# Optimization experiments

Hardware: AMD Instinct MI355X
Metric: run time of the kernel (lower is better)

The kernel has to match this reference:

```python
import jax, jax.numpy as jnp
import numpy as np

EPS = 1e-5
NEG = jnp.float32(-1e30)


def _mha(q_in, kv, in_w, in_b, out_w, out_b, n_heads, allowed=None):
    # torch nn.MultiheadAttention (batch_first, eval mode)
    B, Nq, D = q_in.shape
    hd = D // n_heads
    wq, wk, wv = jnp.split(in_w, 3, axis=0)
    bq, bk, bv = jnp.split(in_b, 3)
    q = (q_in @ wq.T + bq).reshape(B, Nq, n_heads, hd).transpose(0, 2, 1, 3)
    k = (kv @ wk.T + bk).reshape(B, -1, n_heads, hd).transpose(0, 2, 1, 3)
    v = (kv @ wv.T + bv).reshape(B, -1, n_heads, hd).transpose(0, 2, 1, 3)
    s = jnp.einsum('bhqd,bhkd->bhqk', q, k) / jnp.sqrt(jnp.float32(hd))
    if allowed is not None:
        s = jnp.where(allowed[:, None, :, :], s, NEG)
    a = jax.nn.softmax(s, axis=-1)
    o = jnp.einsum('bhqk,bhkd->bhqd', a, v).transpose(0, 2, 1, 3).reshape(B, Nq, D)
    o = o @ out_w.T + out_b
    if allowed is not None:
        # rows with no allowed keys: torch would NaN; we zero them (deterministic)
        o = jnp.where(allowed.any(-1)[..., None], o, 0.0)
    return o


def _layernorm(x, g, b):
    mu = x.mean(-1, keepdims=True)
    var = ((x - mu) ** 2).mean(-1, keepdims=True)
    return (x - mu) * jax.lax.rsqrt(var + EPS) * g + b


def setup_inputs() -> dict:
    key = jax.random.key(0)
    B, N, D, NH = 128, 128, 512, 8
    ks = jax.random.split(key, 16)
    s = 0.02
    return {
        'H': jax.random.normal(ks[0], (B, N, D), jnp.float32),
        'pred_heads': jax.random.randint(ks[1], (B, N), 0, N, jnp.int32),
        'mask': jnp.ones((B, N), jnp.int32),
        'head_in_w': jax.random.normal(ks[2], (3 * D, D)) * s,
        'head_in_b': jnp.zeros((3 * D,), jnp.float32),
        'head_out_w': jax.random.normal(ks[3], (D, D)) * s,
        'head_out_b': jnp.zeros((D,), jnp.float32),
        'sib_in_w': jax.random.normal(ks[4], (3 * D, D)) * s,
        'sib_in_b': jnp.zeros((3 * D,), jnp.float32),
        'sib_out_w': jax.random.normal(ks[5], (D, D)) * s,
        'sib_out_b': jnp.zeros((D,), jnp.float32),
        'child_w': jax.random.normal(ks[6], (D, 2 * D)) * s,
        'child_b': jnp.zeros((D,), jnp.float32),
        'gate_w': jax.random.normal(ks[7], (D, 4 * D)) * s,
        'gate_b': jnp.zeros((D,), jnp.float32),
        'trans_w': jax.random.normal(ks[8], (D, 4 * D)) * s,
        'trans_b': jnp.zeros((D,), jnp.float32),
        'ln_g': jnp.ones((D,), jnp.float32),
        'ln_b': jnp.zeros((D,), jnp.float32),
    }


def reference(H, pred_heads, mask, head_in_w, head_in_b, head_out_w, head_out_b,
              sib_in_w, sib_in_b, sib_out_w, sib_out_b, child_w, child_b,
              gate_w, gate_b, trans_w, trans_b, ln_g, ln_b):
    B, N, D = H.shape
    NH = 8
    heads = jnp.clip(pred_heads, 0, N - 1)  # [B,N]
    maskb = mask.astype(bool)

    # 1) head message: gather each node's head repr, attend Q=H, K=V=head_repr
    head_repr = jnp.take_along_axis(H, heads[..., None], axis=1)  # [B,N,D]
    head_msg = _mha(H, head_repr, head_in_w, head_in_b, head_out_w, head_out_b, NH)

    # 2) child aggregation: vectorized scatter-add replacing the Python loop.
    # loop runs d in [1, length) with mask a prefix -> valid = mask & (d >= 1)
    valid = maskb & (jnp.arange(N) >= 1)  # [B,N]
    contrib = H * valid[..., None].astype(H.dtype)
    flat_idx = (jnp.arange(B)[:, None] * N + heads).reshape(-1)
    child_sum = jnp.zeros((B * N, D), H.dtype).at[flat_idx].add(
        contrib.reshape(B * N, D)).reshape(B, N, D)
    child_count = jnp.zeros((B * N,), H.dtype).at[flat_idx].add(
        valid.reshape(-1).astype(H.dtype)).reshape(B, N, 1)
    child_avg = child_sum / jnp.maximum(child_count, 1.0)
    child_msg = jax.nn.gelu(
        jnp.concatenate([H, child_avg], -1) @ child_w.T + child_b,
        approximate=False)

    # 3) sibling attention (N <= 128 branch): same head, not self, both masked-in
    same_head = heads[:, :, None] == heads[:, None, :]
    eye = jnp.eye(N, dtype=bool)[None]
    allowed = same_head & ~eye & maskb[:, None, :] & maskb[:, :, None]
    sib_msg = _mha(H, H, sib_in_w, sib_in_b, sib_out_w, sib_out_b, NH, allowed=allowed)

    # 4) gated fusion + residual + layernorm
    combined = jnp.concatenate([H, head_msg, child_msg, sib_msg], -1)
    gate = jax.nn.sigmoid(combined @ gate_w.T + gate_b)
    update = jax.nn.gelu(combined @ trans_w.T + trans_b, approximate=False)
    return _layernorm(H + gate * update, ln_g, ln_b)
```

## Files before the change

kernel.cpp:

```cpp
#include <hip/hip_runtime.h>
#include <hip/hip_bf16.h>

typedef __bf16 bf16x8 __attribute__((ext_vector_type(8)));
typedef float f32x4 __attribute__((ext_vector_type(4)));

__device__ __forceinline__ void gload16(const void* g, void* l) {
  __builtin_amdgcn_global_load_lds(
      (const __attribute__((address_space(1))) unsigned int*)g,
      (__attribute__((address_space(3))) unsigned int*)l, 16, 0, 0);
}

__device__ __forceinline__ float gelu_f(float x) {
  return 0.5f * x * (1.f + erff(x * 0.70710678118654752f));
}
__device__ __forceinline__ float sigmoid_f(float x) {
  return 1.f / (1.f + __expf(-x));
}

template<int EPI>
__global__ __launch_bounds__(512, 2)
void gemm8_kernel(const __hip_bfloat16* __restrict__ A0, int lda0,
                  const __hip_bfloat16* __restrict__ A1, int lda1,
                  const __hip_bfloat16* __restrict__ A2, int lda2,
                  int ks1, int ks2,
                  const __hip_bfloat16* __restrict__ B, int ldb,
                  const float* __restrict__ bias,
                  const float* __restrict__ fvec,
                  const float* __restrict__ flags,
                  void* __restrict__ C, int ldc, int K)
{
  extern __shared__ __align__(16) char lds[];
  const int t = threadIdx.x;
  const int l = t & 63;
  const int w = t >> 6;
  const int l15 = l & 15, lg = (l >> 4) & 3;
  const int orig = blockIdx.y * gridDim.x + blockIdx.x;
  const int nwg = gridDim.x * gridDim.y;
  const int gy = gridDim.y;
  const int xcd = orig & 7, rk = orig >> 3, q = nwg >> 3, r = nwg & 7;
  const int bid = (xcd < r ? xcd * (q + 1) : r * (q + 1) + (xcd - r) * q) + rk;
  const int m0 = (bid % gy) * 256;
  const int n0 = (bid / gy) * 256;

  const int srow = t >> 2;
  const int kc8 = ((t & 3) ^ ((t >> 3) & 3)) * 8;
  const int mbase = (w >> 2) * 128;
  const int nbase = (w & 3) * 64;
  const int swz = (l15 >> 1) & 3;
  const int kslot = (lg ^ swz) * 8;
  int aoff[8], boff[4];
#pragma unroll
  for (int mf = 0; mf < 8; ++mf) aoff[mf] = (mbase + mf * 16 + l15) * 32 + kslot;
#pragma unroll
  for (int nf = 0; nf < 4; ++nf) boff[nf] = (nbase + nf * 16 + l15) * 32 + kslot;

  auto segA = [&](int k0, const __hip_bfloat16*& Ap, int& ldA, int& krel) {
    if (k0 >= ks2)      { Ap = A2; ldA = lda2; krel = k0 - ks2; }
    else if (k0 >= ks1) { Ap = A1; ldA = lda1; krel = k0 - ks1; }
    else                { Ap = A0; ldA = lda0; krel = k0; }
  };
  auto stageA = [&](int buf, const __hip_bfloat16* Ap, int ldA, int krel) {
    char* base = lds + buf * 32768 + t * 16;
    gload16(Ap + (size_t)(m0 + srow) * ldA + krel + kc8, base);
    gload16(Ap + (size_t)(m0 + 128 + srow) * ldA + krel + kc8, base + 8192);
  };
  auto stageB = [&](int buf, int k0) {
    char* base = lds + buf * 32768 + 16384 + t * 16;
    gload16(B + (size_t)(n0 + srow) * ldb + k0 + kc8, base);
    gload16(B + (size_t)(n0 + 128 + srow) * ldb + k0 + kc8, base + 8192);
  };

  f32x4 acc[8][4] = {};
  const int NT = K >> 5;

#pragma unroll 1
  for (int pt = 0; pt < 3; ++pt) {
    const __hip_bfloat16* Ap; int ldA, krel;
    segA(pt * 32, Ap, ldA, krel);
    stageA(pt, Ap, ldA, krel);
    stageB(pt, pt * 32);
  }
  asm volatile("s_waitcnt vmcnt(8)" ::: "memory");
  __builtin_amdgcn_s_barrier();
  __builtin_amdgcn_sched_barrier(0);

#pragma unroll 1
  for (int tt = 0; tt < NT; ++tt) {
    const int buf = tt & 3;
    const __hip_bfloat16* As = (const __hip_bfloat16*)(lds + buf * 32768);
    const __hip_bfloat16* Bs = (const __hip_bfloat16*)(lds + buf * 32768 + 16384);
    const int pf = tt + 3;
    const bool do_pf = pf < NT;
    const int pbuf = pf & 3;
    const __hip_bfloat16* Ap = A0; int ldA = lda0, krel = 0;
    if (do_pf) segA(pf * 32, Ap, ldA, krel);

    bf16x8 bv[4], av[4];
#pragma unroll
    for (int nf = 0; nf < 4; ++nf) bv[nf] = *(const bf16x8*)(Bs + boff[nf]);
#pragma unroll
    for (int mf = 0; mf < 4; ++mf) av[mf] = *(const bf16x8*)(As + aoff[mf]);
    if (do_pf) stageA(pbuf, Ap, ldA, krel);
    __builtin_amdgcn_s_setprio(1);
#pragma unroll
    for (int mf = 0; mf < 4; ++mf)
#pragma unroll
      for (int nf = 0; nf < 4; ++nf)
        acc[mf][nf] = __builtin_amdgcn_mfma_f32_16x16x32_bf16(av[mf], bv[nf], acc[mf][nf], 0, 0, 0);
    __builtin_amdgcn_s_setprio(0);

#pragma unroll
    for (int mf = 0; mf < 4; ++mf) av[mf] = *(const bf16x8*)(As + aoff[mf + 4]);
    if (do_pf) stageB(pbuf, pf * 32);
    __builtin_amdgcn_s_setprio(1);
#pragma unroll
    for (int mf = 0; mf < 4; ++mf)
#pragma unroll
      for (int nf = 0; nf < 4; ++nf)
        acc[mf + 4][nf] = __builtin_amdgcn_mfma_f32_16x16x32_bf16(av[mf], bv[nf], acc[mf + 4][nf], 0, 0, 0);
    __builtin_amdgcn_s_setprio(0);

    __builtin_amdgcn_sched_barrier(0);
    if (tt + 3 < NT)      asm volatile("s_waitcnt vmcnt(8)" ::: "memory");
    else if (tt + 2 < NT) asm volatile("s_waitcnt vmcnt(4)" ::: "memory");
    else if (tt + 1 < NT) asm volatile("s_waitcnt vmcnt(0)" ::: "memory");
    if (tt + 1 < NT) {
      __builtin_amdgcn_s_barrier();
      __builtin_amdgcn_sched_barrier(0);
    }
  }

  if (EPI == 2) {
#pragma unroll
    for (int mf = 0; mf < 8; ++mf) {
#pragma unroll
      for (int nh = 0; nh < 2; ++nh) {
        const int nf = nh * 2;
        const int sc = n0 + nbase + nf * 16;
        const float bg = bias[sc + l15], bt = bias[sc + 16 + l15];
        const float fg = fvec[sc + l15], ft = fvec[sc + 16 + l15];
        const int ocol = (sc >> 5) * 16 + l15;
#pragma unroll
        for (int j = 0; j < 4; ++j) {
          const int row = m0 + mbase + mf * 16 + lg * 4 + j;
          const float flg = flags[row];
          float g  = acc[mf][nf][j]     + bg + flg * fg;
          float tv = acc[mf][nf + 1][j] + bt + flg * ft;
          ((float*)C)[(size_t)row * ldc + ocol] = sigmoid_f(g) * gelu_f(tv);
        }
      }
    }
    return;
  }
#pragma unroll
  for (int mf = 0; mf < 8; ++mf)
#pragma unroll
    for (int nf = 0; nf < 4; ++nf) {
      const int col = n0 + nbase + nf * 16 + l15;
      const float bc = bias ? bias[col] : 0.f;
#pragma unroll
      for (int j = 0; j < 4; ++j) {
        const int row = m0 + mbase + mf * 16 + lg * 4 + j;
        ((__hip_bfloat16*)C)[(size_t)row * ldc + col] =
            __float2bfloat16(acc[mf][nf][j] + bc);
      }
    }
}

template<int EPI, bool OBF16>
__global__ __launch_bounds__(256)
void gemm_kernel(const __hip_bfloat16* __restrict__ A0, int lda0,
                 const __hip_bfloat16* __restrict__ A1, int lda1,
                 const __hip_bfloat16* __restrict__ A2, int lda2,
                 int ks1, int ks2,
                 const __hip_bfloat16* __restrict__ B, int ldb,
                 const float* __restrict__ bias,
                 const float* __restrict__ fvec,
                 const float* __restrict__ flags,
                 void* __restrict__ C, int ldc, int K)
{
  __shared__ __align__(16) __hip_bfloat16 As[128 * 32];
  __shared__ __align__(16) __hip_bfloat16 Bs[128 * 32];
  const int t = threadIdx.x;
  const int l = t & 63, w = t >> 6;
  const int gx = gridDim.x;
  int bid = blockIdx.y * gx + blockIdx.x;
  {
    const int nwg = gx * gridDim.y;
    const int xcd = bid & 7, rk = bid >> 3, q = nwg >> 3, r = nwg & 7;
    bid = (xcd < r ? xcd * (q + 1) : r * (q + 1) + (xcd - r) * q) + rk;
  }
  const int m0 = (bid / gx) * 128, n0 = (bid % gx) * 128;
  const int wm = (w >> 1) * 64, wn = (w & 1) * 64;
  const int l15 = l & 15, lg = l >> 4;

  const int r0 = t >> 2;
  const int kk0 = ((t & 3) ^ ((t >> 3) & 3)) * 8;
  char* lA = (char*)As + t * 16;
  char* lB = (char*)Bs + t * 16;
  const size_t boff1 = (size_t)(n0 + r0) * ldb + kk0;
  const size_t boff2 = (size_t)(n0 + r0 + 64) * ldb + kk0;

  int aoffR[4], boffR[4];
#pragma unroll
  for (int i = 0; i < 4; ++i) {
    const int ra = wm + i * 16 + l15;
    aoffR[i] = ra * 32 + ((lg ^ ((ra >> 1) & 3)) * 8);
    const int rb = wn + i * 16 + l15;
    boffR[i] = rb * 32 + ((lg ^ ((rb >> 1) & 3)) * 8);
  }
  f32x4 acc[4][4] = {};

#pragma unroll 1
  for (int seg = 0; seg < 3; ++seg) {
    const __hip_bfloat16* Ap;
    int ldA, kb, ke;
    if (seg == 0)      { Ap = A0; ldA = lda0; kb = 0;   ke = ks1; }
    else if (seg == 1) { Ap = A1; ldA = lda1; kb = ks1; ke = ks2; }
    else               { Ap = A2; ldA = lda2; kb = ks2; ke = K;   }
    if (kb >= ke) continue;
    const size_t aoff1 = (size_t)(m0 + r0) * ldA + kk0;
    const size_t aoff2 = (size_t)(m0 + r0 + 64) * ldA + kk0;
    for (int k0 = kb; k0 < ke; k0 += 32) {
      const int kr = k0 - kb;
      gload16(Ap + aoff1 + kr, lA);
      gload16(Ap + aoff2 + kr, lA + 4096);
      gload16(B + boff1 + k0, lB);
      gload16(B + boff2 + k0, lB + 4096);
      __syncthreads();
      bf16x8 af[4], bfr[4];
#pragma unroll
      for (int i = 0; i < 4; ++i) {
        af[i]  = *(const bf16x8*)((const __hip_bfloat16*)As + aoffR[i]);
        bfr[i] = *(const bf16x8*)((const __hip_bfloat16*)Bs + boffR[i]);
      }
#pragma unroll
      for (int mi = 0; mi < 4; ++mi)
#pragma unroll
        for (int ni = 0; ni < 4; ++ni)
          acc[mi][ni] = __builtin_amdgcn_mfma_f32_16x16x32_bf16(af[mi], bfr[ni], acc[mi][ni], 0, 0, 0);
      __syncthreads();
    }
  }

#pragma unroll
  for (int mi = 0; mi < 4; ++mi)
#pragma unroll
    for (int ni = 0; ni < 4; ++ni) {
      const int col = n0 + wn + ni * 16 + l15;
      const float bc = bias ? bias[col] : 0.f;
#pragma unroll
      for (int j = 0; j < 4; ++j) {
        const int row = m0 + wm + mi * 16 + lg * 4 + j;
        float v = acc[mi][ni][j] + bc;
        if (EPI == 1) v = gelu_f(v);
        if (OBF16) ((__hip_bfloat16*)C)[(size_t)row * ldc + col] = __float2bfloat16(v);
        else       ((float*)C)[(size_t)row * ldc + col] = v;
      }
    }
}

template<bool SIB>
__global__ __launch_bounds__(256)
void attn_kernel(const __hip_bfloat16* __restrict__ QKV,
                 const int* __restrict__ pred_heads,
                 const int* __restrict__ mask,
                 __hip_bfloat16* __restrict__ Oout, int ldo,
                 float* __restrict__ flags,
                 int qofs)
{
  __shared__ __align__(16) __hip_bfloat16 smem[128 * 128];
  __shared__ __align__(16) __hip_bfloat16 Vt[64 * 128];
  __shared__ int hs[128];
  __shared__ int mk[128];
  const int b = blockIdx.x >> 3, h = blockIdx.x & 7;
  const int t = threadIdx.x, l = t & 63, w = t >> 6;
  const int l15 = l & 15, lg = l >> 4;
  __hip_bfloat16* Qs = smem;
  __hip_bfloat16* Ks = smem + 128 * 64;

  if (t < 128) {
    int hh = pred_heads[b * 128 + t];
    hh = hh < 0 ? 0 : (hh > 127 ? 127 : hh);
    hs[t] = hh;
    mk[t] = mask[b * 128 + t];
  }
  __syncthreads();
  const size_t tb = (size_t)b * 128 * 3072;
  const int co = qofs + h * 64;
#pragma unroll
  for (int it = 0; it < 4; ++it) {
    const int idx = it * 256 + t;
    const int row = idx >> 3;
    const int c8 = (idx & 7) * 8;
    const int sl = ((c8 >> 3) ^ (row & 7)) * 8;
    *(uint4*)(Qs + row * 64 + sl) = *(const uint4*)(QKV + tb + (size_t)row * 3072 + co + c8);
    const int krow = SIB ? row : hs[row];
    *(uint4*)(Ks + row * 64 + sl) = *(const uint4*)(QKV + tb + (size_t)krow * 3072 + co + 512 + c8);
    uint4 vv = *(const uint4*)(QKV + tb + (size_t)krow * 3072 + co + 1024 + c8);
    const __hip_bfloat16* vp = (const __hip_bfloat16*)&vv;
#pragma unroll
    for (int u = 0; u < 8; ++u) {
      const int d = c8 + u;
      Vt[d * 128 + (((row >> 3) ^ (d & 7)) * 8) + (row & 7)] = vp[u];
    }
  }
  __syncthreads();

  const int r0 = w * 32;
  f32x4 s[2][8] = {};
  const int x7 = l15 & 7;
#pragma unroll
  for (int ks = 0; ks < 2; ++ks) {
    const int sl = ((ks * 4 + lg) ^ x7) * 8;
    bf16x8 qa0 = *(const bf16x8*)(Qs + (r0 + l15) * 64 + sl);
    bf16x8 qa1 = *(const bf16x8*)(Qs + (r0 + 16 + l15) * 64 + sl);
#pragma unroll
    for (int nj = 0; nj < 8; ++nj) {
      bf16x8 kb = *(const bf16x8*)(Ks + (nj * 16 + l15) * 64 + sl);
      s[0][nj] = __builtin_amdgcn_mfma_f32_16x16x32_bf16(qa0, kb, s[0][nj], 0, 0, 0);
      s[1][nj] = __builtin_amdgcn_mfma_f32_16x16x32_bf16(qa1, kb, s[1][nj], 0, 0, 0);
    }
  }
  const float scale = 0.125f;
  float inv_sum[2][4];
#pragma unroll
  for (int mi = 0; mi < 2; ++mi) {
#pragma unroll
    for (int j = 0; j < 4; ++j) {
      const int row = r0 + mi * 16 + lg * 4 + j;
      float mx = -1e30f;
#pragma unroll
      for (int nj = 0; nj < 8; ++nj) {
        float v = s[mi][nj][j] * scale;
        bool ok = true;
        if (SIB) {
          int c = nj * 16 + l15;
          ok = (hs[row] == hs[c]) && (row != c) && mk[row] && mk[c];
        }
        mx = fmaxf(mx, ok ? v : -1e30f);
      }
#pragma unroll
      for (int m = 1; m < 16; m <<= 1) mx = fmaxf(mx, __shfl_xor(mx, m));
      float sum = 0.f;
#pragma unroll
      for (int nj = 0; nj < 8; ++nj) {
        float v = s[mi][nj][j] * scale;
        bool ok = true;
        if (SIB) {
          int c = nj * 16 + l15;
          ok = (hs[row] == hs[c]) && (row != c) && mk[row] && mk[c];
        }
        float p = ok ? __expf(v - mx) : 0.f;
        s[mi][nj][j] = p;
        sum += p;
      }
#pragma unroll
      for (int m = 1; m < 16; m <<= 1) sum += __shfl_xor(sum, m);
      inv_sum[mi][j] = sum > 0.f ? 1.f / sum : 0.f;
    }
  }
  __syncthreads();
#pragma unroll
  for (int mi = 0; mi < 2; ++mi)
#pragma unroll
    for (int nj = 0; nj < 8; ++nj)
#pragma unroll
      for (int j = 0; j < 4; ++j) {
        const int rr = r0 + mi * 16 + lg * 4 + j;
        const int cc = nj * 16 + l15;
        smem[rr * 128 + (((cc >> 3) ^ (rr & 7)) * 8) + (cc & 7)] = __float2bfloat16(s[mi][nj][j]);
      }
  __syncthreads();

  f32x4 o[2][4] = {};
#pragma unroll
  for (int js = 0; js < 4; ++js) {
    const int slot = js * 4 + lg;
    const int slp = (slot ^ x7) * 8;
    bf16x8 pa0 = *(const bf16x8*)(smem + (r0 + l15) * 128 + slp);
    bf16x8 pa1 = *(const bf16x8*)(smem + (r0 + 16 + l15) * 128 + slp);
#pragma unroll
    for (int dj = 0; dj < 4; ++dj) {
      bf16x8 vb = *(const bf16x8*)(Vt + (dj * 16 + l15) * 128 + slp);
      o[0][dj] = __builtin_amdgcn_mfma_f32_16x16x32_bf16(pa0, vb, o[0][dj], 0, 0, 0);
      o[1][dj] = __builtin_amdgcn_mfma_f32_16x16x32_bf16(pa1, vb, o[1][dj], 0, 0, 0);
    }
  }
  const int hb = h * 64;
#pragma unroll
  for (int mi = 0; mi < 2; ++mi)
#pragma unroll
    for (int dj = 0; dj < 4; ++dj)
#pragma unroll
      for (int j = 0; j < 4; ++j) {
        const int row = r0 + mi * 16 + lg * 4 + j;
        const int dc = dj * 16 + l15;
        const float val = o[mi][dj][j] * inv_sum[mi][j];
        Oout[(size_t)(b * 128 + row) * ldo + hb + dc] = __float2bfloat16(val);
      }
  if (SIB && h == 0 && l15 == 0) {
#pragma unroll
    for (int mi = 0; mi < 2; ++mi)
#pragma unroll
      for (int j = 0; j < 4; ++j) {
        const int row = r0 + mi * 16 + lg * 4 + j;
        flags[b * 128 + row] = inv_sum[mi][j] > 0.f ? 1.f : 0.f;
      }
  }
}

__global__ __launch_bounds__(256)
void child_kernel(const float* __restrict__ H,
                  const int* __restrict__ pred_heads,
                  const int* __restrict__ mask,
                  __hip_bfloat16* __restrict__ Cavg)
{
  __shared__ float sum[128 * 64];
  __shared__ int cnt[128];
  __shared__ int hsl[128];
  __shared__ int vld[128];
  const int t = threadIdx.x;
  const int b = blockIdx.y, ch = blockIdx.x;
#pragma unroll
  for (int u = 0; u < 32; ++u) sum[u * 256 + t] = 0.f;
  if (t < 128) {
    int hh = pred_heads[b * 128 + t];
    hh = hh < 0 ? 0 : (hh > 127 ? 127 : hh);
    hsl[t] = hh;
    vld[t] = (mask[b * 128 + t] != 0) && (t >= 1);
    cnt[t] = 0;
  }
  __syncthreads();
  if (t < 128 && vld[t]) atomicAdd(&cnt[hsl[t]], 1);
  __syncthreads();
  const int c = t & 63;
  const int isub = t >> 6;
  for (int ii = 0; ii < 32; ++ii) {
    int i = ii * 4 + isub;
    if (vld[i]) atomicAdd(&sum[hsl[i] * 64 + c], H[((size_t)b * 128 + i) * 512 + ch * 64 + c]);
  }
  __syncthreads();
#pragma unroll
  for (int u = 0; u < 32; ++u) {
    int idx = u * 256 + t;
    int p = idx >> 6, cc = idx & 63;
    float avg = sum[idx] / fmaxf((float)cnt[p], 1.f);
    Cavg[((size_t)b * 128 + p) * 512 + ch * 64 + cc] = __float2bfloat16(avg);
  }
}

__global__ void conv_all_kernel(const float* __restrict__ s0, const float* __restrict__ s1,
                                const float* __restrict__ s2, const float* __restrict__ s3,
                                __hip_bfloat16* __restrict__ d0, __hip_bfloat16* __restrict__ d1,
                                __hip_bfloat16* __restrict__ d2, __hip_bfloat16* __restrict__ d3)
{
  int gid = blockIdx.x * 256 + threadIdx.x;
  const float* s; __hip_bfloat16* d; int i;
  if      (gid <  196608) { s = s0; d = d0; i = gid; }
  else if (gid <  393216) { s = s1; d = d1; i = gid - 196608; }
  else if (gid <  524288) { s = s2; d = d2; i = gid - 393216; }
  else                    { s = s3; d = d3; i = gid - 524288; }
  i *= 4;
  float4 v = *(const float4*)(s + i);
  union { __hip_bfloat16 h[4]; uint2 u; } p;
  p.h[0] = __float2bfloat16(v.x); p.h[1] = __float2bfloat16(v.y);
  p.h[2] = __float2bfloat16(v.z); p.h[3] = __float2bfloat16(v.w);
  *(uint2*)(d + i) = p.u;
}

__global__ void convT_kernel(const float* __restrict__ a, const float* __restrict__ b,
                             __hip_bfloat16* __restrict__ ta, __hip_bfloat16* __restrict__ tb)
{
  int idx = blockIdx.x * 256 + threadIdx.x;
  const float* s = a; __hip_bfloat16* d = ta;
  if (idx >= 262144) { s = b; d = tb; idx -= 262144; }
  int i = idx >> 9, j = idx & 511;
  d[i * 512 + j] = __float2bfloat16(s[(size_t)j * 512 + i]);
}

__global__ void build_gt_kernel(const float* __restrict__ gw, const float* __restrict__ tw,
                                const float* __restrict__ gb, const float* __restrict__ tb,
                                __hip_bfloat16* __restrict__ Wf, __hip_bfloat16* __restrict__ Whin,
                                __hip_bfloat16* __restrict__ Wsin, float* __restrict__ bias)
{
  int idx = blockIdx.x * 256 + threadIdx.x;
  int s = idx >> 11, c = idx & 2047;
  int q = s >> 5, r = s & 31;
  float v = (r < 16) ? gw[(size_t)(q * 16 + r) * 2048 + c]
                     : tw[(size_t)(q * 16 + r - 16) * 2048 + c];
  __hip_bfloat16 hv = __float2bfloat16(v);
  if      (c <  512) Wf[(size_t)s * 2048 + c] = hv;
  else if (c < 1024) Whin[(size_t)s * 512 + (c - 512)] = hv;
  else if (c < 1536) Wf[(size_t)s * 2048 + (c - 512)] = hv;
  else               Wsin[(size_t)s * 512 + (c - 1536)] = hv;
  if (c == 0) bias[s] = (r < 16) ? gb[q * 16 + r] : tb[q * 16 + r - 16];
}

__global__ __launch_bounds__(256)
void foldbias_kernel(const __hip_bfloat16* __restrict__ Whin, const __hip_bfloat16* __restrict__ Wsin,
                     const float* __restrict__ hob, const float* __restrict__ sob,
                     float* __restrict__ bias_gt, float* __restrict__ fvec)
{
  const int s = blockIdx.x * 256 + threadIdx.x;
  float a = 0.f, c = 0.f;
  for (int j = 0; j < 512; j += 8) {
    bf16x8 wh = *(const bf16x8*)(Whin + (size_t)s * 512 + j);
    bf16x8 wsv = *(const bf16x8*)(Wsin + (size_t)s * 512 + j);
#pragma unroll
    for (int u = 0; u < 8; ++u) {
      a += (float)wh[u] * hob[j + u];
      c += (float)wsv[u] * sob[j + u];
    }
  }
  bias_gt[s] += a;
  fvec[s] = c;
}

__global__ __launch_bounds__(64)
void ln_kernel(const float* __restrict__ H, const float* __restrict__ U,
               const float* __restrict__ g, const float* __restrict__ bta,
               float* __restrict__ out)
{
  const int row = blockIdx.x, l = threadIdx.x;
  const size_t hb = (size_t)row * 512;
  float x[8];
  float sum = 0.f;
#pragma unroll
  for (int u = 0; u < 8; ++u) {
    int d = u * 64 + l;
    float val = H[hb + d] + U[hb + d];
    x[u] = val; sum += val;
  }
#pragma unroll
  for (int m = 32; m; m >>= 1) sum += __shfl_xor(sum, m);
  float mean = sum * (1.f / 512.f);
  float vs = 0.f;
#pragma unroll
  for (int u = 0; u < 8; ++u) { float d0 = x[u] - mean; vs += d0 * d0; }
#pragma unroll
  for (int m = 32; m; m >>= 1) vs += __shfl_xor(vs, m);
  float rstd = rsqrtf(vs * (1.f / 512.f) + 1e-5f);
#pragma unroll
  for (int u = 0; u < 8; ++u) {
    int d = u * 64 + l;
    out[hb + d] = (x[u] - mean) * rstd * g[d] + bta[d];
  }
}

extern "C" void kernel_launch(void* const* d_in, const int* in_sizes, int n_in,
                              void* d_out, int out_size, void* d_ws, size_t ws_size,
                              hipStream_t stream)
{
  (void)in_sizes; (void)n_in; (void)out_size; (void)ws_size;
  const float* H      = (const float*)d_in[0];
  const int*  pred    = (const int*)d_in[1];
  const int*  maskp   = (const int*)d_in[2];
  const float* hin_w  = (const float*)d_in[3];
  const float* hin_b  = (const float*)d_in[4];
  const float* hout_w = (const float*)d_in[5];
  const float* hout_b = (const float*)d_in[6];
  const float* sin_w  = (const float*)d_in[7];
  const float* sin_b  = (const float*)d_in[8];
  const float* sout_w = (const float*)d_in[9];
  const float* sout_b = (const float*)d_in[10];
  const float* ch_w   = (const float*)d_in[11];
  const float* ch_b   = (const float*)d_in[12];
  const float* g_w    = (const float*)d_in[13];
  const float* g_b    = (const float*)d_in[14];
  const float* t_w    = (const float*)d_in[15];
  const float* t_b    = (const float*)d_in[16];
  const float* lng    = (const float*)d_in[17];
  const float* lnb    = (const float*)d_in[18];

  char* ws = (char*)d_ws;
  __hip_bfloat16* Wqkv  = (__hip_bfloat16*)(ws + 0);
  __hip_bfloat16* Wch   = (__hip_bfloat16*)(ws + 3145728);
  __hip_bfloat16* Wgt   = (__hip_bfloat16*)(ws + 4194304);
  float* bias_qkv       = (float*)(ws + 8388608);
  float* bias_gt        = (float*)(ws + 8400896);
  float* fvec           = (float*)(ws + 8404992);
  float* flags          = (float*)(ws + 8409088);
  __hip_bfloat16* Hbf   = (__hip_bfloat16*)(ws + 8474624);
  char* QKVr            = ws + 25251840;
  __hip_bfloat16* QKV   = (__hip_bfloat16*)QKVr;
  __hip_bfloat16* Whin  = (__hip_bfloat16*)(QKVr + 0);
  __hip_bfloat16* Wsin  = (__hip_bfloat16*)(QKVr + 1048576);
  __hip_bfloat16* WhoT  = (__hip_bfloat16*)(QKVr + 2097152);
  __hip_bfloat16* WsoT  = (__hip_bfloat16*)(QKVr + 2621440);
  __hip_bfloat16* CHM   = (__hip_bfloat16*)(QKVr + 0);
  float* U              = (float*)(QKVr + 16777216);
  __hip_bfloat16* Cavg  = (__hip_bfloat16*)(QKVr + 50331648);
  __hip_bfloat16* CM2   = (__hip_bfloat16*)(ws + 125915136);

  hipFuncSetAttribute(reinterpret_cast<const void*>(gemm8_kernel<0>),
                      hipFuncAttributeMaxDynamicSharedMemorySize, 131072);
  hipFuncSetAttribute(reinterpret_cast<const void*>(gemm8_kernel<2>),
                      hipFuncAttributeMaxDynamicSharedMemorySize, 131072);

  conv_all_kernel<<<10240, 256, 0, stream>>>(hin_w, sin_w, ch_w, H,
                                             Wqkv, Wqkv + 786432, Wch, Hbf);
  build_gt_kernel<<<8192, 256, 0, stream>>>(g_w, t_w, g_b, t_b, Wgt, Whin, Wsin, bias_gt);
  convT_kernel<<<2048, 256, 0, stream>>>(hout_w, sout_w, WhoT, WsoT);
  foldbias_kernel<<<4, 256, 0, stream>>>(Whin, Wsin, hout_b, sout_b, bias_gt, fvec);
  hipMemcpyAsync(bias_qkv, hin_b, 1536 * 4, hipMemcpyDeviceToDevice, stream);
  hipMemcpyAsync(bias_qkv + 1536, sin_b, 1536 * 4, hipMemcpyDeviceToDevice, stream);

  gemm_kernel<0, true><<<dim3(4, 8), 256, 0, stream>>>(
      Whin, 512, Whin, 512, Whin, 512, 512, 512, WhoT, 512,
      (const float*)nullptr, (const float*)nullptr, (const float*)nullptr,
      (void*)(Wgt + 1024), 2048, 512);
  gemm_kernel<0, true><<<dim3(4, 8), 256, 0, stream>>>(
      Wsin, 512, Wsin, 512, Wsin, 512, 512, 512, WsoT, 512,
      (const float*)nullptr, (const float*)nullptr, (const float*)nullptr,
      (void*)(Wgt + 1536), 2048, 512);

  gemm8_kernel<0><<<dim3(12, 64), 512, 131072, stream>>>(
      Hbf, 512, Hbf, 512, Hbf, 512, 512, 512, Wqkv, 512,
      bias_qkv, (const float*)nullptr, (const float*)nullptr,
      (void*)QKV, 3072, 512);

  attn_kernel<false><<<1024, 256, 0, stream>>>(QKV, pred, maskp, CM2, 1024, flags, 0);
  attn_kernel<true><<<1024, 256, 0, stream>>>(QKV, pred, maskp, CM2 + 512, 1024, flags, 1536);

  child_kernel<<<dim3(8, 128), 256, 0, stream>>>(H, pred, maskp, Cavg);
  gemm_kernel<1, true><<<dim3(4, 128), 256, 0, stream>>>(
      Hbf, 512, Cavg, 512, Cavg, 512, 512, 1024, Wch, 1024,
      ch_b, (const float*)nullptr, (const float*)nullptr,
      (void*)CHM, 512, 1024);

  gemm8_kernel<2><<<dim3(4, 64), 512, 131072, stream>>>(
      Hbf, 512, CHM, 512, CM2, 1024, 512, 1024, Wgt, 2048,
      bias_gt, fvec, flags, (void*)U, 512, 2048);

  ln_kernel<<<16384, 64, 0, stream>>>(H, U, lng, lnb, (float*)d_out);
}
```

Before: 488.5 us.

## Merge prep and attention launches, store gated update in bf16, vectorize layernorm

```diff
diff --git a/kernel.cpp b/kernel.cpp
--- a/kernel.cpp
+++ b/kernel.cpp
@@ -146,7 +146,8 @@
           const float flg = flags[row];
           float g  = acc[mf][nf][j]     + bg + flg * fg;
           float tv = acc[mf][nf + 1][j] + bt + flg * ft;
-          ((float*)C)[(size_t)row * ldc + ocol] = sigmoid_f(g) * gelu_f(tv);
+          ((__hip_bfloat16*)C)[(size_t)row * ldc + ocol] =
+              __float2bfloat16(sigmoid_f(g) * gelu_f(tv));
         }
       }
     }
@@ -260,20 +261,22 @@
     }
 }
 
-template<bool SIB>
 __global__ __launch_bounds__(256)
 void attn_kernel(const __hip_bfloat16* __restrict__ QKV,
                  const int* __restrict__ pred_heads,
                  const int* __restrict__ mask,
-                 __hip_bfloat16* __restrict__ Oout, int ldo,
-                 float* __restrict__ flags,
-                 int qofs)
+                 __hip_bfloat16* __restrict__ Oout,
+                 float* __restrict__ flags)
 {
   __shared__ __align__(16) __hip_bfloat16 smem[128 * 128];
   __shared__ __align__(16) __hip_bfloat16 Vt[64 * 128];
   __shared__ int hs[128];
   __shared__ int mk[128];
-  const int b = blockIdx.x >> 3, h = blockIdx.x & 7;
+  const bool SIB = blockIdx.x >= 1024;
+  const int bh = blockIdx.x & 1023;
+  const int b = bh >> 3, h = bh & 7;
+  const int qofs = SIB ? 1536 : 0;
+  __hip_bfloat16* Ob = Oout + (SIB ? 512 : 0);
   const int t = threadIdx.x, l = t & 63, w = t >> 6;
   const int l15 = l & 15, lg = l >> 4;
   __hip_bfloat16* Qs = smem;
@@ -397,7 +400,7 @@
         const int row = r0 + mi * 16 + lg * 4 + j;
         const int dc = dj * 16 + l15;
         const float val = o[mi][dj][j] * inv_sum[mi][j];
-        Oout[(size_t)(b * 128 + row) * ldo + hb + dc] = __float2bfloat16(val);
+        Ob[(size_t)(b * 128 + row) * 1024 + hb + dc] = __float2bfloat16(val);
       }
   if (SIB && h == 0 && l15 == 0) {
 #pragma unroll
@@ -411,7 +414,7 @@
 }
 
 __global__ __launch_bounds__(256)
-void child_kernel(const float* __restrict__ H,
+void child_kernel(const __hip_bfloat16* __restrict__ Hbf,
                   const int* __restrict__ pred_heads,
                   const int* __restrict__ mask,
                   __hip_bfloat16* __restrict__ Cavg)
@@ -438,7 +441,9 @@
   const int isub = t >> 6;
   for (int ii = 0; ii < 32; ++ii) {
     int i = ii * 4 + isub;
-    if (vld[i]) atomicAdd(&sum[hsl[i] * 64 + c], H[((size_t)b * 128 + i) * 512 + ch * 64 + c]);
+    if (vld[i])
+      atomicAdd(&sum[hsl[i] * 64 + c],
+                __bfloat162float(Hbf[((size_t)b * 128 + i) * 512 + ch * 64 + c]));
   }
   __syncthreads();
 #pragma unroll
@@ -450,51 +455,49 @@
   }
 }
 
-__global__ void conv_all_kernel(const float* __restrict__ s0, const float* __restrict__ s1,
-                                const float* __restrict__ s2, const float* __restrict__ s3,
-                                __hip_bfloat16* __restrict__ d0, __hip_bfloat16* __restrict__ d1,
-                                __hip_bfloat16* __restrict__ d2, __hip_bfloat16* __restrict__ d3)
+__global__ void prep_kernel(const float* __restrict__ hin_w, const float* __restrict__ sin_w,
+                            const float* __restrict__ ch_w, const float* __restrict__ H,
+                            __hip_bfloat16* __restrict__ Wqkv, __hip_bfloat16* __restrict__ Wch,
+                            __hip_bfloat16* __restrict__ Hbf,
+                            const float* __restrict__ gw, const float* __restrict__ tw,
+                            const float* __restrict__ gb, const float* __restrict__ tb,
+                            __hip_bfloat16* __restrict__ Wf, __hip_bfloat16* __restrict__ Whin,
+                            __hip_bfloat16* __restrict__ Wsin, float* __restrict__ bias,
+                            const float* __restrict__ hout_w, const float* __restrict__ sout_w,
+                            __hip_bfloat16* __restrict__ WhoT, __hip_bfloat16* __restrict__ WsoT)
 {
   int gid = blockIdx.x * 256 + threadIdx.x;
-  const float* s; __hip_bfloat16* d; int i;
-  if      (gid <  196608) { s = s0; d = d0; i = gid; }
-  else if (gid <  393216) { s = s1; d = d1; i = gid - 196608; }
-  else if (gid <  524288) { s = s2; d = d2; i = gid - 393216; }
-  else                    { s = s3; d = d3; i = gid - 524288; }
-  i *= 4;
-  float4 v = *(const float4*)(s + i);
-  union { __hip_bfloat16 h[4]; uint2 u; } p;
-  p.h[0] = __float2bfloat16(v.x); p.h[1] = __float2bfloat16(v.y);
-  p.h[2] = __float2bfloat16(v.z); p.h[3] = __float2bfloat16(v.w);
-  *(uint2*)(d + i) = p.u;
-}
-
-__global__ void convT_kernel(const float* __restrict__ a, const float* __restrict__ b,
-                             __hip_bfloat16* __restrict__ ta, __hip_bfloat16* __restrict__ tb)
-{
-  int idx = blockIdx.x * 256 + threadIdx.x;
-  const float* s = a; __hip_bfloat16* d = ta;
-  if (idx >= 262144) { s = b; d = tb; idx -= 262144; }
-  int i = idx >> 9, j = idx & 511;
-  d[i * 512 + j] = __float2bfloat16(s[(size_t)j * 512 + i]);
-}
-
-__global__ void build_gt_kernel(const float* __restrict__ gw, const float* __restrict__ tw,
-                                const float* __restrict__ gb, const float* __restrict__ tb,
-                                __hip_bfloat16* __restrict__ Wf, __hip_bfloat16* __restrict__ Whin,
-                                __hip_bfloat16* __restrict__ Wsin, float* __restrict__ bias)
-{
-  int idx = blockIdx.x * 256 + threadIdx.x;
-  int s = idx >> 11, c = idx & 2047;
-  int q = s >> 5, r = s & 31;
-  float v = (r < 16) ? gw[(size_t)(q * 16 + r) * 2048 + c]
-                     : tw[(size_t)(q * 16 + r - 16) * 2048 + c];
-  __hip_bfloat16 hv = __float2bfloat16(v);
-  if      (c <  512) Wf[(size_t)s * 2048 + c] = hv;
-  else if (c < 1024) Whin[(size_t)s * 512 + (c - 512)] = hv;
-  else if (c < 1536) Wf[(size_t)s * 2048 + (c - 512)] = hv;
-  else               Wsin[(size_t)s * 512 + (c - 1536)] = hv;
-  if (c == 0) bias[s] = (r < 16) ? gb[q * 16 + r] : tb[q * 16 + r - 16];
+  if (gid < 2621440) {
+    const float* s; __hip_bfloat16* d; int i;
+    if      (gid <  196608) { s = hin_w; d = Wqkv;          i = gid; }
+    else if (gid <  393216) { s = sin_w; d = Wqkv + 786432; i = gid - 196608; }
+    else if (gid <  524288) { s = ch_w;  d = Wch;           i = gid - 393216; }
+    else                    { s = H;     d = Hbf;           i = gid - 524288; }
+    i *= 4;
+    float4 v = *(const float4*)(s + i);
+    union { __hip_bfloat16 h[4]; uint2 u; } p;
+    p.h[0] = __float2bfloat16(v.x); p.h[1] = __float2bfloat16(v.y);
+    p.h[2] = __float2bfloat16(v.z); p.h[3] = __float2bfloat16(v.w);
+    *(uint2*)(d + i) = p.u;
+  } else if (gid < 4718592) {
+    int idx = gid - 2621440;
+    int s = idx >> 11, c = idx & 2047;
+    int q = s >> 5, r = s & 31;
+    float v = (r < 16) ? gw[(size_t)(q * 16 + r) * 2048 + c]
+                       : tw[(size_t)(q * 16 + r - 16) * 2048 + c];
+    __hip_bfloat16 hv = __float2bfloat16(v);
+    if      (c <  512) Wf[(size_t)s * 2048 + c] = hv;
+    else if (c < 1024) Whin[(size_t)s * 512 + (c - 512)] = hv;
+    else if (c < 1536) Wf[(size_t)s * 2048 + (c - 512)] = hv;
+    else               Wsin[(size_t)s * 512 + (c - 1536)] = hv;
+    if (c == 0) bias[s] = (r < 16) ? gb[q * 16 + r] : tb[q * 16 + r - 16];
+  } else {
+    int idx = gid - 4718592;
+    const float* s = hout_w; __hip_bfloat16* d = WhoT;
+    if (idx >= 262144) { s = sout_w; d = WsoT; idx -= 262144; }
+    int i = idx >> 9, j = idx & 511;
+    d[i * 512 + j] = __float2bfloat16(s[(size_t)j * 512 + i]);
+  }
 }
 
 __global__ __launch_bounds__(256)
@@ -518,34 +521,48 @@
 }
 
 __global__ __launch_bounds__(64)
-void ln_kernel(const float* __restrict__ H, const float* __restrict__ U,
+void ln_kernel(const float* __restrict__ H, const __hip_bfloat16* __restrict__ U,
                const float* __restrict__ g, const float* __restrict__ bta,
                float* __restrict__ out)
 {
   const int row = blockIdx.x, l = threadIdx.x;
   const size_t hb = (size_t)row * 512;
+  const int c0 = l * 8;
+  float4 h0 = *(const float4*)(H + hb + c0);
+  float4 h1 = *(const float4*)(H + hb + c0 + 4);
+  bf16x8 uv = *(const bf16x8*)(U + hb + c0);
   float x[8];
+  x[0] = h0.x + (float)uv[0]; x[1] = h0.y + (float)uv[1];
+  x[2] = h0.z + (float)uv[2]; x[3] = h0.w + (float)uv[3];
+  x[4] = h1.x + (float)uv[4]; x[5] = h1.y + (float)uv[5];
+  x[6] = h1.z + (float)uv[6]; x[7] = h1.w + (float)uv[7];
   float sum = 0.f;
 #pragma unroll
-  for (int u = 0; u < 8; ++u) {
-    int d = u * 64 + l;
-    float val = H[hb + d] + U[hb + d];
-    x[u] = val; sum += val;
-  }
+  for (int u = 0; u < 8; ++u) sum += x[u];
 #pragma unroll
   for (int m = 32; m; m >>= 1) sum += __shfl_xor(sum, m);
-  float mean = sum * (1.f / 512.f);
+  const float mean = sum * (1.f / 512.f);
   float vs = 0.f;
 #pragma unroll
   for (int u = 0; u < 8; ++u) { float d0 = x[u] - mean; vs += d0 * d0; }
 #pragma unroll
   for (int m = 32; m; m >>= 1) vs += __shfl_xor(vs, m);
-  float rstd = rsqrtf(vs * (1.f / 512.f) + 1e-5f);
-#pragma unroll
-  for (int u = 0; u < 8; ++u) {
-    int d = u * 64 + l;
-    out[hb + d] = (x[u] - mean) * rstd * g[d] + bta[d];
-  }
+  const float rstd = rsqrtf(vs * (1.f / 512.f) + 1e-5f);
+  float4 g0 = *(const float4*)(g + c0);
+  float4 g1 = *(const float4*)(g + c0 + 4);
+  float4 b0 = *(const float4*)(bta + c0);
+  float4 b1 = *(const float4*)(bta + c0 + 4);
+  float4 o0, o1;
+  o0.x = (x[0] - mean) * rstd * g0.x + b0.x;
+  o0.y = (x[1] - mean) * rstd * g0.y + b0.y;
+  o0.z = (x[2] - mean) * rstd * g0.z + b0.z;
+  o0.w = (x[3] - mean) * rstd * g0.w + b0.w;
+  o1.x = (x[4] - mean) * rstd * g1.x + b1.x;
+  o1.y = (x[5] - mean) * rstd * g1.y + b1.y;
+  o1.z = (x[6] - mean) * rstd * g1.z + b1.z;
+  o1.w = (x[7] - mean) * rstd * g1.w + b1.w;
+  *(float4*)(out + hb + c0) = o0;
+  *(float4*)(out + hb + c0 + 4) = o1;
 }
 
 extern "C" void kernel_launch(void* const* d_in, const int* in_sizes, int n_in,
@@ -589,7 +606,7 @@
   __hip_bfloat16* WhoT  = (__hip_bfloat16*)(QKVr + 2097152);
   __hip_bfloat16* WsoT  = (__hip_bfloat16*)(QKVr + 2621440);
   __hip_bfloat16* CHM   = (__hip_bfloat16*)(QKVr + 0);
-  float* U              = (float*)(QKVr + 16777216);
+  __hip_bfloat16* U     = (__hip_bfloat16*)(QKVr + 16777216);
   __hip_bfloat16* Cavg  = (__hip_bfloat16*)(QKVr + 50331648);
   __hip_bfloat16* CM2   = (__hip_bfloat16*)(ws + 125915136);
 
@@ -598,10 +615,9 @@
   hipFuncSetAttribute(reinterpret_cast<const void*>(gemm8_kernel<2>),
                       hipFuncAttributeMaxDynamicSharedMemorySize, 131072);
 
-  conv_all_kernel<<<10240, 256, 0, stream>>>(hin_w, sin_w, ch_w, H,
-                                             Wqkv, Wqkv + 786432, Wch, Hbf);
-  build_gt_kernel<<<8192, 256, 0, stream>>>(g_w, t_w, g_b, t_b, Wgt, Whin, Wsin, bias_gt);
-  convT_kernel<<<2048, 256, 0, stream>>>(hout_w, sout_w, WhoT, WsoT);
+  prep_kernel<<<20480, 256, 0, stream>>>(hin_w, sin_w, ch_w, H, Wqkv, Wch, Hbf,
+                                         g_w, t_w, g_b, t_b, Wgt, Whin, Wsin, bias_gt,
+                                         hout_w, sout_w, WhoT, WsoT);
   foldbias_kernel<<<4, 256, 0, stream>>>(Whin, Wsin, hout_b, sout_b, bias_gt, fvec);
   hipMemcpyAsync(bias_qkv, hin_b, 1536 * 4, hipMemcpyDeviceToDevice, stream);
   hipMemcpyAsync(bias_qkv + 1536, sin_b, 1536 * 4, hipMemcpyDeviceToDevice, stream);
@@ -620,10 +636,9 @@
       bias_qkv, (const float*)nullptr, (const float*)nullptr,
       (void*)QKV, 3072, 512);
 
-  attn_kernel<false><<<1024, 256, 0, stream>>>(QKV, pred, maskp, CM2, 1024, flags, 0);
-  attn_kernel<true><<<1024, 256, 0, stream>>>(QKV, pred, maskp, CM2 + 512, 1024, flags, 1536);
-
-  child_kernel<<<dim3(8, 128), 256, 0, stream>>>(H, pred, maskp, Cavg);
+  attn_kernel<<<2048, 256, 0, stream>>>(QKV, pred, maskp, CM2, flags);
+
+  child_kernel<<<dim3(8, 128), 256, 0, stream>>>(Hbf, pred, maskp, Cavg);
   gemm_kernel<1, true><<<dim3(4, 128), 256, 0, stream>>>(
       Hbf, 512, Cavg, 512, Cavg, 512, 512, 1024, Wch, 1024,
       ch_b, (const float*)nullptr, (const float*)nullptr,
```

After: 509.0 us. 4.2% more time.
